# Kernel tuning notes

Hardware: AMD Instinct MI355X
Metric: run time of the kernel (lower is better)

Reference implementation:

```python
import jax, jax.numpy as jnp
import numpy as np
from jax import lax

ALPHABET = 64
E = 1024   # embedding_dim == output_dim == HIDDEN
H = 1024
MSG_LEN = 20
BOS = ALPHABET          # 64
PAD = ALPHABET + 1      # 65
EOS = 0
B = 4096


def setup_inputs() -> dict:
    key = jax.random.key(0)
    ks = jax.random.split(key, 12)
    def u(k, shape, s):
        return jax.random.uniform(k, shape, jnp.float32, -s, s)
    sE = 1.0 / np.sqrt(E)
    sH = 1.0 / np.sqrt(H)
    embed = jax.random.normal(ks[0], (ALPHABET + 2, E), jnp.float32)
    embed = embed.at[PAD].set(0.0)  # padding_idx row is zero
    return dict(
        encoded=jax.random.normal(ks[1], (B, E), jnp.float32),
        embed=embed,
        W_ih=u(ks[2], (4 * H, E), sH), W_hh=u(ks[3], (4 * H, H), sH),
        b_ih=u(ks[4], (4 * H,), sH), b_hh=u(ks[5], (4 * H,), sH),
        W_cell=u(ks[6], (E, E), sE), b_cell=u(ks[7], (E,), sE),
        W_hid=u(ks[8], (E, E), sE), b_hid=u(ks[9], (E,), sE),
        W_act=u(ks[10], (ALPHABET, E), sE), b_act=u(ks[11], (ALPHABET,), sE),
    )


def reference(encoded, embed, W_ih, W_hh, b_ih, b_hh,
              W_cell, b_cell, W_hid, b_hid, W_act, b_act):
    b = encoded.shape[0]
    # torch passes state=(cell, hidden) to nn.LSTM, which reads (h0, c0):
    h0 = encoded @ W_cell.T + b_cell
    c0 = encoded @ W_hid.T + b_hid
    last0 = jnp.full((b,), BOS, jnp.int32)
    stopped0 = jnp.zeros((b,), bool)
    keys = jax.random.split(jax.random.key(42), MSG_LEN)
    bias = b_ih + b_hh

    def step(carry, k):
        h, c, last, stopped = carry
        # embedding lookup; zero the pad row (padding_idx semantics)
        x = embed[last] * (last != PAD)[:, None].astype(embed.dtype)
        gates = x @ W_ih.T + h @ W_hh.T + bias          # [b, 4H], gate order i,f,g,o
        i, f, g, o = jnp.split(gates, 4, axis=-1)
        c2 = jax.nn.sigmoid(f) * c + jax.nn.sigmoid(i) * jnp.tanh(g)
        h2 = jax.nn.sigmoid(o) * jnp.tanh(c2)
        logits = h2 @ W_act.T + b_act                   # [b, ALPHABET]
        action = jax.random.categorical(k, logits)      # training-mode sample
        logp = jax.nn.log_softmax(logits)
        live = (~stopped).astype(logits.dtype)
        ent = -jnp.sum(jnp.exp(logp) * logp, axis=-1) * live
        lp = jnp.take_along_axis(logp, action[:, None], axis=1)[:, 0] * live
        action = jnp.where(stopped, PAD, action).astype(jnp.int32)
        stopped2 = stopped | (action == EOS)
        return (h2, c2, action, stopped2), (action, lp, ent)

    _, (msg, lps, ents) = lax.scan(step, (h0, c0, last0, stopped0), keys)
    msg = msg.T          # [b, MSG_LEN]
    log_probs = lps.T    # [b, MSG_LEN]
    ents = ents.T        # [b, MSG_LEN]
    message_len = jnp.sum(msg != PAD, axis=1, keepdims=True)  # count of non-pad symbols
    entropy = jnp.sum(ents, axis=1, keepdims=True) / message_len.astype(ents.dtype)
    return entropy, log_probs, msg, message_len
```

## Files before the change

kernel.cpp:

```cpp
#include <hip/hip_runtime.h>
#include <stdint.h>

#define ALPHA 64
#define EDIM 1024
#define G4 4096
#define BATCH 4096
#define TLEN 20
#define BOS_TOK 64
#define PAD_TOK 65
#define EOS_TOK 0

__device__ __forceinline__ void threefry2x32(uint32_t k0, uint32_t k1,
                                             uint32_t& x0, uint32_t& x1) {
  uint32_t ks[3] = {k0, k1, k0 ^ k1 ^ 0x1BD11BDAu};
  const int rot0[4] = {13, 15, 26, 6};
  const int rot1[4] = {17, 29, 16, 24};
  x0 += ks[0];
  x1 += ks[1];
#pragma unroll
  for (int i = 0; i < 5; ++i) {
    const int* rr = (i & 1) ? rot1 : rot0;
#pragma unroll
    for (int j = 0; j < 4; ++j) {
      x0 += x1;
      x1 = (x1 << rr[j]) | (x1 >> (32 - rr[j]));
      x1 ^= x0;
    }
    x0 += ks[(i + 1) % 3];
    x1 += ks[(i + 2) % 3] + (uint32_t)(i + 1);
  }
}

__global__ void init_kernel(uint32_t* __restrict__ keyA, uint32_t* __restrict__ keyB,
                            int* __restrict__ last, int* __restrict__ stopped,
                            double* __restrict__ ent_sum, int* __restrict__ len_sum) {
  int i = blockIdx.x * 256 + threadIdx.x;
  if (i < BATCH) {
    last[i] = BOS_TOK;
    stopped[i] = 0;
    ent_sum[i] = 0.0;
    len_sum[i] = 0;
  }
  if (i < TLEN) {
    uint32_t x0 = 0u, x1 = (uint32_t)i;
    threefry2x32(0u, 42u, x0, x1);
    keyA[i] = x0;
    keyB[i] = x1;
  }
}

__global__ void transpose_wact(const float* __restrict__ W, float* __restrict__ Wt) {
  int i = blockIdx.x * 256 + threadIdx.x;
  if (i < ALPHA * EDIM) {
    int a = i >> 10, k = i & 1023;
    Wt[(size_t)k * ALPHA + a] = W[i];
  }
}

__global__ __launch_bounds__(256) void gemm_nt0(
    const float* __restrict__ A, const float* __restrict__ Bw, float* __restrict__ C,
    int M, int N, int K, const float* __restrict__ bias1) {
  __shared__ float As[16][132];
  __shared__ float Bs[16][132];
  const int t = threadIdx.x;
  const int bm = blockIdx.y * 128;
  const int bn = blockIdx.x * 128;
  const int tx = t & 15, ty = t >> 4;

  float acc[8][8];
#pragma unroll
  for (int i = 0; i < 8; ++i)
#pragma unroll
    for (int j = 0; j < 8; ++j) acc[i][j] = 0.0f;

  const int sr = t >> 1;
  const int sc = (t & 1) << 3;
  const float* ap = A + (size_t)(bm + sr) * K + sc;
  const float* bp = Bw + (size_t)(bn + sr) * K + sc;
  const bool aok = (bm + sr) < M;

  for (int k0 = 0; k0 < K; k0 += 16) {
    float4 av0 = {0.f, 0.f, 0.f, 0.f}, av1 = {0.f, 0.f, 0.f, 0.f};
    if (aok) {
      av0 = *(const float4*)(ap + k0);
      av1 = *(const float4*)(ap + k0 + 4);
    }
    float4 bv0 = *(const float4*)(bp + k0);
    float4 bv1 = *(const float4*)(bp + k0 + 4);
    __syncthreads();
    As[sc + 0][sr] = av0.x; As[sc + 1][sr] = av0.y; As[sc + 2][sr] = av0.z; As[sc + 3][sr] = av0.w;
    As[sc + 4][sr] = av1.x; As[sc + 5][sr] = av1.y; As[sc + 6][sr] = av1.z; As[sc + 7][sr] = av1.w;
    Bs[sc + 0][sr] = bv0.x; Bs[sc + 1][sr] = bv0.y; Bs[sc + 2][sr] = bv0.z; Bs[sc + 3][sr] = bv0.w;
    Bs[sc + 4][sr] = bv1.x; Bs[sc + 5][sr] = bv1.y; Bs[sc + 6][sr] = bv1.z; Bs[sc + 7][sr] = bv1.w;
    __syncthreads();
#pragma unroll
    for (int k = 0; k < 16; ++k) {
      float4 a0 = *(const float4*)&As[k][ty * 4];
      float4 a1 = *(const float4*)&As[k][ty * 4 + 64];
      float4 b0 = *(const float4*)&Bs[k][tx * 4];
      float4 b1 = *(const float4*)&Bs[k][tx * 4 + 64];
      float ar[8] = {a0.x, a0.y, a0.z, a0.w, a1.x, a1.y, a1.z, a1.w};
      float br[8] = {b0.x, b0.y, b0.z, b0.w, b1.x, b1.y, b1.z, b1.w};
#pragma unroll
      for (int i = 0; i < 8; ++i)
#pragma unroll
        for (int j = 0; j < 8; ++j) acc[i][j] = fmaf(ar[i], br[j], acc[i][j]);
    }
  }

#pragma unroll
  for (int i = 0; i < 8; ++i) {
    int mG = bm + ty * 4 + (i & 3) + ((i >> 2) << 6);
    if (mG >= M) continue;
#pragma unroll
    for (int j = 0; j < 8; ++j) {
      int nG = bn + tx * 4 + (j & 3) + ((j >> 2) << 6);
      float v = acc[i][j];
      if (bias1) v = __fadd_rn(v, bias1[nG]);
      C[(size_t)mG * N + nG] = v;
    }
  }
}

__global__ __launch_bounds__(256) void gemm_lstm_fused(
    const float* __restrict__ A, const float* __restrict__ Bw,
    const float* __restrict__ eg, const int* __restrict__ lastIdx,
    const float* __restrict__ b_ih, const float* __restrict__ b_hh,
    float* __restrict__ hN, float* __restrict__ cst) {
  __shared__ float As[16][132];
  __shared__ float Bs[16][132];
  const int t = threadIdx.x;
  const int bm = blockIdx.y * 128;
  const int j0 = blockIdx.x * 32;
  const int tx = t & 15, ty = t >> 4;

  float acc[8][8];
#pragma unroll
  for (int i = 0; i < 8; ++i)
#pragma unroll
    for (int j = 0; j < 8; ++j) acc[i][j] = 0.0f;

  const int sr = t >> 1;
  const int sc = (t & 1) << 3;
  const float* ap = A + (size_t)(bm + sr) * EDIM + sc;
  const float* bp = Bw + (size_t)((sr & 3) * EDIM + j0 + (sr >> 2)) * EDIM + sc;

  float4 av0 = *(const float4*)(ap);
  float4 av1 = *(const float4*)(ap + 4);
  float4 bv0 = *(const float4*)(bp);
  float4 bv1 = *(const float4*)(bp + 4);

  for (int k0 = 0; k0 < EDIM; k0 += 16) {
    __syncthreads();
    As[sc + 0][sr] = av0.x; As[sc + 1][sr] = av0.y; As[sc + 2][sr] = av0.z; As[sc + 3][sr] = av0.w;
    As[sc + 4][sr] = av1.x; As[sc + 5][sr] = av1.y; As[sc + 6][sr] = av1.z; As[sc + 7][sr] = av1.w;
    Bs[sc + 0][sr] = bv0.x; Bs[sc + 1][sr] = bv0.y; Bs[sc + 2][sr] = bv0.z; Bs[sc + 3][sr] = bv0.w;
    Bs[sc + 4][sr] = bv1.x; Bs[sc + 5][sr] = bv1.y; Bs[sc + 6][sr] = bv1.z; Bs[sc + 7][sr] = bv1.w;
    if (k0 + 16 < EDIM) {
      av0 = *(const float4*)(ap + k0 + 16);
      av1 = *(const float4*)(ap + k0 + 20);
      bv0 = *(const float4*)(bp + k0 + 16);
      bv1 = *(const float4*)(bp + k0 + 20);
    }
    __syncthreads();
#pragma unroll
    for (int k = 0; k < 16; ++k) {
      float4 a0 = *(const float4*)&As[k][ty * 4];
      float4 a1 = *(const float4*)&As[k][ty * 4 + 64];
      float4 b0 = *(const float4*)&Bs[k][tx * 4];
      float4 b1 = *(const float4*)&Bs[k][tx * 4 + 64];
      float ar[8] = {a0.x, a0.y, a0.z, a0.w, a1.x, a1.y, a1.z, a1.w};
      float br[8] = {b0.x, b0.y, b0.z, b0.w, b1.x, b1.y, b1.z, b1.w};
#pragma unroll
      for (int i = 0; i < 8; ++i)
#pragma unroll
        for (int j = 0; j < 8; ++j) acc[i][j] = fmaf(ar[i], br[j], acc[i][j]);
    }
  }

#pragma unroll
  for (int i = 0; i < 8; ++i) {
    const int row = bm + ty * 4 + (i & 3) + ((i >> 2) << 6);
    const float* egrow = eg + (size_t)lastIdx[row] * G4;
#pragma unroll
    for (int jj = 0; jj < 2; ++jj) {
      const int jg = j0 + tx + jj * 16;
      float gv[4];
#pragma unroll
      for (int g = 0; g < 4; ++g) {
        const int n = g * EDIM + jg;
        const float bsum = __fadd_rn(b_ih[n], b_hh[n]);
        gv[g] = __fadd_rn(__fadd_rn(egrow[n], acc[i][jj * 4 + g]), bsum);
      }
      const size_t idx = (size_t)row * EDIM + jg;
      float cc = cst[idx];
      float si = 1.0f / (__fadd_rn(1.0f, expf(-gv[0])));
      float sf = 1.0f / (__fadd_rn(1.0f, expf(-gv[1])));
      float so = 1.0f / (__fadd_rn(1.0f, expf(-gv[3])));
      float c2 = __fadd_rn(__fmul_rn(sf, cc), __fmul_rn(si, tanhf(gv[2])));
      float h2 = __fmul_rn(so, tanhf(c2));
      cst[idx] = c2;
      hN[idx] = h2;
    }
  }
}

__global__ __launch_bounds__(256) void logits_sample(
    const float* __restrict__ h, const float* __restrict__ Wt,
    const float* __restrict__ b_act,
    const uint32_t* __restrict__ keyA, const uint32_t* __restrict__ keyB, int tstep,
    int* __restrict__ last, int* __restrict__ stopped,
    double* __restrict__ ent_sum, int* __restrict__ len_sum,
    float* __restrict__ out_lp, float* __restrict__ out_msg) {
  __shared__ float Ws[64][64];
  __shared__ float Hs[8][64];
  const int tid = threadIdx.x;
  const int wave = tid >> 6;
  const int lane = tid & 63;
  const int rowBase = blockIdx.x * 8;

  float acc0 = 0.0f, acc1 = 0.0f;
  for (int kp = 0; kp < EDIM; kp += 64) {
    __syncthreads();
    {
      const float4* src = (const float4*)(Wt + (size_t)kp * ALPHA);
      float4* dst = (float4*)&Ws[0][0];
#pragma unroll
      for (int q = 0; q < 4; ++q) dst[tid + q * 256] = src[tid + q * 256];
    }
    if (tid < 128) {
      int rr = tid >> 4;
      int cc = (tid & 15) << 2;
      *(float4*)&Hs[rr][cc] = *(const float4*)(h + (size_t)(rowBase + rr) * EDIM + kp + cc);
    }
    __syncthreads();
#pragma unroll
    for (int kk = 0; kk < 64; ++kk) {
      float w = Ws[kk][lane];
      acc0 = fmaf(Hs[wave * 2 + 0][kk], w, acc0);
      acc1 = fmaf(Hs[wave * 2 + 1][kk], w, acc1);
    }
  }

  const float ba = b_act[lane];
  const uint32_t k0 = keyA[tstep], k1 = keyB[tstep];
  float logitv[2] = {__fadd_rn(acc0, ba), __fadd_rn(acc1, ba)};

#pragma unroll
  for (int rsel = 0; rsel < 2; ++rsel) {
    const int b = rowBase + wave * 2 + rsel;
    const float logit = logitv[rsel];

    uint32_t m = ((uint32_t)b << 6) | (uint32_t)lane;
    uint32_t x0 = 0u, x1 = m;
    threefry2x32(k0, k1, x0, x1);
    uint32_t bits = x0 ^ x1;

    float f = __fsub_rn(__uint_as_float((bits >> 9) | 0x3F800000u), 1.0f);
    const float TINY = 1.17549435e-38f;
    float u = fmaxf(TINY, __fadd_rn(f, TINY));
    float gmb = -logf(-logf(u));
    float z = __fadd_rn(logit, gmb);

    float bv = z;
    int bi = lane;
#pragma unroll
    for (int off = 32; off > 0; off >>= 1) {
      float ov = __shfl_xor(bv, off, 64);
      int oi = __shfl_xor(bi, off, 64);
      if (ov > bv || (ov == bv && oi < bi)) { bv = ov; bi = oi; }
    }

    float mx = logit;
#pragma unroll
    for (int off = 32; off > 0; off >>= 1) mx = fmaxf(mx, __shfl_xor(mx, off, 64));
    float sh = __fsub_rn(logit, mx);
    float e = expf(sh);
    float s = e;
#pragma unroll
    for (int off = 32; off > 0; off >>= 1) s = __fadd_rn(s, __shfl_xor(s, off, 64));
    float ls = logf(s);
    float logp = __fsub_rn(sh, ls);

    float term = __fmul_rn(expf(logp), logp);
    float ts = term;
#pragma unroll
    for (int off = 32; off > 0; off >>= 1) ts = __fadd_rn(ts, __shfl_xor(ts, off, 64));

    float lp_taken = __shfl(logp, bi, 64);

    int st = stopped[b];
    float live = st ? 0.0f : 1.0f;
    int act = st ? PAD_TOK : bi;
    int st2 = (st || act == EOS_TOK) ? 1 : 0;

    if (lane == 0) {
      out_msg[(size_t)b * TLEN + tstep] = (float)act;
      out_lp[(size_t)b * TLEN + tstep] = __fmul_rn(lp_taken, live);
      ent_sum[b] += (double)__fmul_rn(-ts, live);
      len_sum[b] += (act != PAD_TOK) ? 1 : 0;
      last[b] = act;
      stopped[b] = st2;
    }
  }
}

__global__ void finalize_kernel(const double* __restrict__ ent_sum,
                                const int* __restrict__ len_sum,
                                float* __restrict__ out_ent, float* __restrict__ out_len) {
  int b = blockIdx.x * 256 + threadIdx.x;
  if (b < BATCH) {
    out_ent[b] = (float)(ent_sum[b] / (double)len_sum[b]);
    out_len[b] = (float)len_sum[b];
  }
}

extern "C" void kernel_launch(void* const* d_in, const int* in_sizes, int n_in,
                              void* d_out, int out_size, void* d_ws, size_t ws_size,
                              hipStream_t stream) {
  const float* encoded = (const float*)d_in[0];
  const float* embed = (const float*)d_in[1];
  const float* W_ih = (const float*)d_in[2];
  const float* W_hh = (const float*)d_in[3];
  const float* b_ih = (const float*)d_in[4];
  const float* b_hh = (const float*)d_in[5];
  const float* W_cell = (const float*)d_in[6];
  const float* b_cell = (const float*)d_in[7];
  const float* W_hid = (const float*)d_in[8];
  const float* b_hid = (const float*)d_in[9];
  const float* W_act = (const float*)d_in[10];
  const float* b_act = (const float*)d_in[11];

  float* out = (float*)d_out;
  float* out_ent = out;
  float* out_lp = out + BATCH;
  float* out_msg = out + BATCH + BATCH * TLEN;
  float* out_len = out + BATCH + 2 * BATCH * TLEN;

  char* ws = (char*)d_ws;
  size_t off = 0;
  auto alloc = [&](size_t bytes) -> void* {
    void* p = ws + off;
    off = (off + bytes + 255) & ~(size_t)255;
    return p;
  };
  float* h0b = (float*)alloc(sizeof(float) * (size_t)BATCH * EDIM);
  float* h1b = (float*)alloc(sizeof(float) * (size_t)BATCH * EDIM);
  float* c = (float*)alloc(sizeof(float) * (size_t)BATCH * EDIM);
  float* eg = (float*)alloc(sizeof(float) * 66 * G4);
  float* Wt = (float*)alloc(sizeof(float) * EDIM * ALPHA);
  uint32_t* keyA = (uint32_t*)alloc(sizeof(uint32_t) * TLEN);
  uint32_t* keyB = (uint32_t*)alloc(sizeof(uint32_t) * TLEN);
  int* last = (int*)alloc(sizeof(int) * BATCH);
  int* stopped = (int*)alloc(sizeof(int) * BATCH);
  double* ent_s = (double*)alloc(sizeof(double) * BATCH);
  int* len_s = (int*)alloc(sizeof(int) * BATCH);
  (void)ws_size; (void)in_sizes; (void)n_in; (void)out_size;

  init_kernel<<<16, 256, 0, stream>>>(keyA, keyB, last, stopped, ent_s, len_s);
  transpose_wact<<<(ALPHA * EDIM) / 256, 256, 0, stream>>>(W_act, Wt);

  gemm_nt0<<<dim3(32, 1), 256, 0, stream>>>(embed, W_ih, eg, 66, G4, EDIM, nullptr);
  gemm_nt0<<<dim3(8, 32), 256, 0, stream>>>(encoded, W_cell, h0b, BATCH, EDIM, EDIM, b_cell);
  gemm_nt0<<<dim3(8, 32), 256, 0, stream>>>(encoded, W_hid, c, BATCH, EDIM, EDIM, b_hid);

  float* hb[2] = {h0b, h1b};
  for (int t = 0; t < TLEN; ++t) {
    const float* hin = hb[t & 1];
    float* hout = hb[(t & 1) ^ 1];
    gemm_lstm_fused<<<dim3(32, 32), 256, 0, stream>>>(hin, W_hh, eg, last,
                                                      b_ih, b_hh, hout, c);
    logits_sample<<<BATCH / 8, 256, 0, stream>>>(hout, Wt, b_act, keyA, keyB, t,
                                                 last, stopped, ent_s, len_s,
                                                 out_lp, out_msg);
  }
  finalize_kernel<<<16, 256, 0, stream>>>(ent_s, len_s, out_ent, out_len);
}
```

Baseline: 9.638 ms.

## Compact live rows each step and skip GEMM work for stopped sequences

Each step now builds a list of non-stopped batch rows with an atomic counter. The recurrent gate GEMM gathers only those rows, and blocks past the live count exit early. The fused GEMM+LSTM epilogue is split into a gate GEMM that writes a full BATCH×4H gate buffer and a separate pointwise LSTM kernel, and the register prefetch of the next K tile is dropped. The aim is to avoid recurrent matmul work on finished sequences, at the cost of extra gate-buffer memory traffic, more kernel launches and a row gather.

New measurement: 8.879 ms. -7.9%, faster.

```diff
diff --git a/kernel.cpp b/kernel.cpp
--- a/kernel.cpp
+++ b/kernel.cpp
@@ -33,7 +33,8 @@
 
 __global__ void init_kernel(uint32_t* __restrict__ keyA, uint32_t* __restrict__ keyB,
                             int* __restrict__ last, int* __restrict__ stopped,
-                            double* __restrict__ ent_sum, int* __restrict__ len_sum) {
+                            double* __restrict__ ent_sum, int* __restrict__ len_sum,
+                            int* __restrict__ cnt) {
   int i = blockIdx.x * 256 + threadIdx.x;
   if (i < BATCH) {
     last[i] = BOS_TOK;
@@ -46,6 +47,17 @@
     threefry2x32(0u, 42u, x0, x1);
     keyA[i] = x0;
     keyB[i] = x1;
+    cnt[i] = 0;
+  }
+}
+
+__global__ void compact_alive(const int* __restrict__ stopped,
+                              int* __restrict__ aliveIdx, int* __restrict__ cnt,
+                              int t) {
+  int i = blockIdx.x * 256 + threadIdx.x;
+  if (i < BATCH && !stopped[i]) {
+    int p = atomicAdd(&cnt[t], 1);
+    aliveIdx[p] = i;
   }
 }
 
@@ -122,16 +134,18 @@
   }
 }
 
-__global__ __launch_bounds__(256) void gemm_lstm_fused(
-    const float* __restrict__ A, const float* __restrict__ Bw,
+__global__ __launch_bounds__(256) void gemm_gates(
+    const float* __restrict__ A, const float* __restrict__ Bw, float* __restrict__ C,
+    const float* __restrict__ bias1, const float* __restrict__ bias2,
     const float* __restrict__ eg, const int* __restrict__ lastIdx,
-    const float* __restrict__ b_ih, const float* __restrict__ b_hh,
-    float* __restrict__ hN, float* __restrict__ cst) {
+    const int* __restrict__ aliveIdx, const int* __restrict__ aliveCnt) {
+  const int an = *aliveCnt;
+  const int bm = blockIdx.y * 128;
+  if (bm >= an) return;
   __shared__ float As[16][132];
   __shared__ float Bs[16][132];
   const int t = threadIdx.x;
-  const int bm = blockIdx.y * 128;
-  const int j0 = blockIdx.x * 32;
+  const int bn = blockIdx.x * 128;
   const int tx = t & 15, ty = t >> 4;
 
   float acc[8][8];
@@ -142,26 +156,21 @@
 
   const int sr = t >> 1;
   const int sc = (t & 1) << 3;
-  const float* ap = A + (size_t)(bm + sr) * EDIM + sc;
-  const float* bp = Bw + (size_t)((sr & 3) * EDIM + j0 + (sr >> 2)) * EDIM + sc;
-
-  float4 av0 = *(const float4*)(ap);
-  float4 av1 = *(const float4*)(ap + 4);
-  float4 bv0 = *(const float4*)(bp);
-  float4 bv1 = *(const float4*)(bp + 4);
+  const int lp = bm + sr;
+  const int arow = (lp < an) ? aliveIdx[lp] : 0;
+  const float* ap = A + (size_t)arow * EDIM + sc;
+  const float* bp = Bw + (size_t)(bn + sr) * EDIM + sc;
 
   for (int k0 = 0; k0 < EDIM; k0 += 16) {
+    float4 av0 = *(const float4*)(ap + k0);
+    float4 av1 = *(const float4*)(ap + k0 + 4);
+    float4 bv0 = *(const float4*)(bp + k0);
+    float4 bv1 = *(const float4*)(bp + k0 + 4);
     __syncthreads();
     As[sc + 0][sr] = av0.x; As[sc + 1][sr] = av0.y; As[sc + 2][sr] = av0.z; As[sc + 3][sr] = av0.w;
     As[sc + 4][sr] = av1.x; As[sc + 5][sr] = av1.y; As[sc + 6][sr] = av1.z; As[sc + 7][sr] = av1.w;
     Bs[sc + 0][sr] = bv0.x; Bs[sc + 1][sr] = bv0.y; Bs[sc + 2][sr] = bv0.z; Bs[sc + 3][sr] = bv0.w;
     Bs[sc + 4][sr] = bv1.x; Bs[sc + 5][sr] = bv1.y; Bs[sc + 6][sr] = bv1.z; Bs[sc + 7][sr] = bv1.w;
-    if (k0 + 16 < EDIM) {
-      av0 = *(const float4*)(ap + k0 + 16);
-      av1 = *(const float4*)(ap + k0 + 20);
-      bv0 = *(const float4*)(bp + k0 + 16);
-      bv1 = *(const float4*)(bp + k0 + 20);
-    }
     __syncthreads();
 #pragma unroll
     for (int k = 0; k < 16; ++k) {
@@ -180,29 +189,43 @@
 
 #pragma unroll
   for (int i = 0; i < 8; ++i) {
-    const int row = bm + ty * 4 + (i & 3) + ((i >> 2) << 6);
+    const int mlp = bm + ty * 4 + (i & 3) + ((i >> 2) << 6);
+    if (mlp >= an) continue;
+    const int row = aliveIdx[mlp];
     const float* egrow = eg + (size_t)lastIdx[row] * G4;
 #pragma unroll
-    for (int jj = 0; jj < 2; ++jj) {
-      const int jg = j0 + tx + jj * 16;
-      float gv[4];
-#pragma unroll
-      for (int g = 0; g < 4; ++g) {
-        const int n = g * EDIM + jg;
-        const float bsum = __fadd_rn(b_ih[n], b_hh[n]);
-        gv[g] = __fadd_rn(__fadd_rn(egrow[n], acc[i][jj * 4 + g]), bsum);
-      }
-      const size_t idx = (size_t)row * EDIM + jg;
-      float cc = cst[idx];
-      float si = 1.0f / (__fadd_rn(1.0f, expf(-gv[0])));
-      float sf = 1.0f / (__fadd_rn(1.0f, expf(-gv[1])));
-      float so = 1.0f / (__fadd_rn(1.0f, expf(-gv[3])));
-      float c2 = __fadd_rn(__fmul_rn(sf, cc), __fmul_rn(si, tanhf(gv[2])));
-      float h2 = __fmul_rn(so, tanhf(c2));
-      cst[idx] = c2;
-      hN[idx] = h2;
-    }
-  }
+    for (int j = 0; j < 8; ++j) {
+      int nG = bn + tx * 4 + (j & 3) + ((j >> 2) << 6);
+      float bsum = __fadd_rn(bias1[nG], bias2[nG]);
+      float v = __fadd_rn(__fadd_rn(egrow[nG], acc[i][j]), bsum);
+      C[(size_t)row * G4 + nG] = v;
+    }
+  }
+}
+
+__global__ __launch_bounds__(256) void lstm_pointwise(const float* __restrict__ gates,
+                                                      float* __restrict__ h,
+                                                      float* __restrict__ c,
+                                                      const int* __restrict__ aliveIdx,
+                                                      const int* __restrict__ aliveCnt) {
+  int idx = blockIdx.x * 256 + threadIdx.x;
+  int lp = idx >> 10, jj = idx & 1023;
+  if (lp >= *aliveCnt) return;
+  int row = aliveIdx[lp];
+  const float* grow = gates + ((size_t)row << 12);
+  float gi = grow[jj];
+  float gf = grow[jj + 1024];
+  float gg = grow[jj + 2048];
+  float go = grow[jj + 3072];
+  size_t cidx = ((size_t)row << 10) + jj;
+  float cc = c[cidx];
+  float si = 1.0f / (__fadd_rn(1.0f, expf(-gi)));
+  float sf = 1.0f / (__fadd_rn(1.0f, expf(-gf)));
+  float so = 1.0f / (__fadd_rn(1.0f, expf(-go)));
+  float c2 = __fadd_rn(__fmul_rn(sf, cc), __fmul_rn(si, tanhf(gg)));
+  float h2 = __fmul_rn(so, tanhf(c2));
+  c[cidx] = c2;
+  h[cidx] = h2;
 }
 
 __global__ __launch_bounds__(256) void logits_sample(
@@ -344,9 +367,9 @@
     off = (off + bytes + 255) & ~(size_t)255;
     return p;
   };
-  float* h0b = (float*)alloc(sizeof(float) * (size_t)BATCH * EDIM);
-  float* h1b = (float*)alloc(sizeof(float) * (size_t)BATCH * EDIM);
+  float* h = (float*)alloc(sizeof(float) * (size_t)BATCH * EDIM);
   float* c = (float*)alloc(sizeof(float) * (size_t)BATCH * EDIM);
+  float* gates = (float*)alloc(sizeof(float) * (size_t)BATCH * G4);
   float* eg = (float*)alloc(sizeof(float) * 66 * G4);
   float* Wt = (float*)alloc(sizeof(float) * EDIM * ALPHA);
   uint32_t* keyA = (uint32_t*)alloc(sizeof(uint32_t) * TLEN);
@@ -355,22 +378,24 @@
   int* stopped = (int*)alloc(sizeof(int) * BATCH);
   double* ent_s = (double*)alloc(sizeof(double) * BATCH);
   int* len_s = (int*)alloc(sizeof(int) * BATCH);
+  int* aliveIdx = (int*)alloc(sizeof(int) * BATCH);
+  int* cnt = (int*)alloc(sizeof(int) * TLEN);
   (void)ws_size; (void)in_sizes; (void)n_in; (void)out_size;
 
-  init_kernel<<<16, 256, 0, stream>>>(keyA, keyB, last, stopped, ent_s, len_s);
+  init_kernel<<<16, 256, 0, stream>>>(keyA, keyB, last, stopped, ent_s, len_s, cnt);
   transpose_wact<<<(ALPHA * EDIM) / 256, 256, 0, stream>>>(W_act, Wt);
 
   gemm_nt0<<<dim3(32, 1), 256, 0, stream>>>(embed, W_ih, eg, 66, G4, EDIM, nullptr);
-  gemm_nt0<<<dim3(8, 32), 256, 0, stream>>>(encoded, W_cell, h0b, BATCH, EDIM, EDIM, b_cell);
+  gemm_nt0<<<dim3(8, 32), 256, 0, stream>>>(encoded, W_cell, h, BATCH, EDIM, EDIM, b_cell);
   gemm_nt0<<<dim3(8, 32), 256, 0, stream>>>(encoded, W_hid, c, BATCH, EDIM, EDIM, b_hid);
 
-  float* hb[2] = {h0b, h1b};
   for (int t = 0; t < TLEN; ++t) {
-    const float* hin = hb[t & 1];
-    float* hout = hb[(t & 1) ^ 1];
-    gemm_lstm_fused<<<dim3(32, 32), 256, 0, stream>>>(hin, W_hh, eg, last,
-                                                      b_ih, b_hh, hout, c);
-    logits_sample<<<BATCH / 8, 256, 0, stream>>>(hout, Wt, b_act, keyA, keyB, t,
+    compact_alive<<<16, 256, 0, stream>>>(stopped, aliveIdx, cnt, t);
+    gemm_gates<<<dim3(32, 32), 256, 0, stream>>>(h, W_hh, gates, b_ih, b_hh,
+                                                 eg, last, aliveIdx, cnt + t);
+    lstm_pointwise<<<(BATCH * EDIM) / 256, 256, 0, stream>>>(gates, h, c,
+                                                             aliveIdx, cnt + t);
+    logits_sample<<<BATCH / 8, 256, 0, stream>>>(h, Wt, b_act, keyA, keyB, t,
                                                  last, stopped, ent_s, len_s,
                                                  out_lp, out_msg);
   }
```
